# Optimization experiments

Measured on AMD Instinct MI355X. Metric: run time of the kernel, lower is better.

The kernel has to match this reference:

```python
import jax, jax.numpy as jnp
import numpy as np

N = 111          # brain regions
K_POOL = 100     # ceil(0.9 * 111), hard-coded by inter_channel_adj shape
C_ASSIGN = 56    # int(0.5 * 112)
B = 2048
E = 4000

LEFT = np.array([6,5,55,1,98,71,73,77,63,96,79,15,104,4,25,23,41,43,45,17,61,65,59,57,86,21,35,37,39,94,110,3,69,81,84,100,102,106,47,27,75,2,67,19,49,31,33,108,51,53,88,90,92,29,0])
RIGHT = np.array([13,12,54,8,97,70,72,76,62,95,78,14,103,11,24,22,40,42,44,16,60,64,58,56,85,20,34,36,38,93,109,10,68,80,83,99,101,105,46,26,74,9,66,18,48,30,32,107,50,52,87,89,91,28,7])

def _gcn(x, A, W, b):
    # PyG GCNConv: out = D^-1/2 (A + I) D^-1/2 (x W) + b, deg from weighted adj + self loops
    Ah = A + jnp.eye(N, dtype=x.dtype)
    d = Ah.sum(axis=1)
    dis = jnp.where(d > 0, jax.lax.rsqrt(d), 0.0).astype(x.dtype)
    return (dis[:, None] * Ah * dis[None, :]) @ (x @ W) + b

def _forward_batch(features, edge_attr, edge_index, params):
    src, dst = edge_index[0], edge_index[1]
    inL = jnp.zeros((N,), bool).at[jnp.asarray(LEFT)].set(True)
    inR = jnp.zeros((N,), bool).at[jnp.asarray(RIGHT)].set(True)
    # subgraph(): keep edges with both endpoints in hemisphere (masking == removal for weighted GCN)
    ml = (inL[src] & inL[dst]).astype(features.dtype)
    mr = (inR[src] & inR[dst]).astype(features.dtype)
    (W_l1, b_l1, W_r1, b_r1, W_l2, b_l2, W_r2, b_r2, W_g1, b_g1,
     W_rel, b_rel, W_root, W_c0, W_c1, W_c2, b_c) = params
    lrelu = lambda z: jax.nn.leaky_relu(z, 0.01)
    no_diag = 1.0 - jnp.eye(N, dtype=features.dtype)

    def one(x, ew):
        dense = lambda w: jnp.zeros((N, N), x.dtype).at[dst, src].add(w)  # A[target, source]
        A_l, A_r, A_g = dense(ew * ml), dense(ew * mr), dense(ew)
        hl = lrelu(_gcn(x, A_l, W_l1, b_l1))
        hr = lrelu(_gcn(x, A_r, W_r1, b_r1))
        h1 = jnp.zeros((N, 64), x.dtype).at[LEFT].set(hl[LEFT]).at[RIGHT].set(hr[RIGHT])
        hl2 = lrelu(_gcn(h1, A_l, W_l2, b_l2))
        hr2 = lrelu(_gcn(h1, A_r, W_r2, b_r2))
        h2 = jnp.zeros((N, 20), x.dtype).at[LEFT].set(hl2[LEFT]).at[RIGHT].set(hr2[RIGHT])
        h2 = lrelu(_gcn(h2, A_g, W_g1, b_g1))
        # SAGPooling: GraphConv score (aggr=add with edge weights) -> tanh -> top-100
        score = jnp.tanh((A_g @ h2) @ W_rel + b_rel + h2 @ W_root)[:, 0]
        perm = jnp.argsort(-score)[:K_POOL]               # descending-score order (PyG topk)
        pooled = h2[perm] * score[perm][:, None]          # [100, 20]
        # filter_adj: relabel surviving edges into 0..99 (ChebConv still runs on 111 nodes)
        mapping = jnp.full((N,), -1, jnp.int32).at[perm].set(jnp.arange(K_POOL, dtype=jnp.int32))
        ms, mt = mapping[src], mapping[dst]
        keepb = (ms >= 0) & (mt >= 0)
        A_p = jnp.zeros((N, N), x.dtype).at[jnp.where(keepb, mt, 0), jnp.where(keepb, ms, 0)].add(keepb.astype(x.dtype)) * no_diag
        # ChebConv K=3, sym norm, lambda_max=2 -> scaled Laplacian = -D^-1/2 A D^-1/2 (zero diag)
        dC = A_p.sum(axis=0)
        disC = jnp.where(dC > 0, jax.lax.rsqrt(dC), 0.0).astype(x.dtype)
        Lh = -(disC[:, None] * A_p * disC[None, :])
        Tx1 = Lh @ h2
        Tx2 = 2.0 * (Lh @ Tx1) - h2
        ass = jax.nn.softmax(h2 @ W_c0 + Tx1 @ W_c1 + Tx2 @ W_c2 + b_c, axis=-1)  # [111, 56]
        s2 = jax.nn.softmax(ass, axis=-1)  # dense_diff_pool softmaxes again (faithful)
        Hc = s2.T @ h2                     # [56, 20]
        # python loop: rows of ass for nodes in perm with index < 110, ascending node order
        sp = jnp.sort(perm)
        inter = ass[sp] * (sp < 110)[:, None].astype(x.dtype)  # [100, 56]
        return (pooled + inter @ Hc).reshape(1, -1)             # [1, 2000]

    return jax.vmap(one)(features, edge_attr)

def setup_inputs() -> dict:
    key = jax.random.key(0)
    ks = jax.random.split(key, 16)
    w = lambda k, shape: 0.1 * jax.random.normal(k, shape, jnp.float32)
    inp = {
        'features': jax.random.normal(ks[0], (B, N, N), jnp.float32),
        'edge_attr': jax.random.uniform(ks[1], (B, E), jnp.float32),
        'adj': jax.random.uniform(ks[2], (B, N, N), jnp.float32),
        'edge_index': jax.random.randint(ks[3], (2, E), 0, N),
        'W_l1': w(ks[4], (N, 64)), 'b_l1': jnp.zeros((64,), jnp.float32),
        'W_r1': w(ks[5], (N, 64)), 'b_r1': jnp.zeros((64,), jnp.float32),
        'W_l2': w(ks[6], (64, 20)), 'b_l2': jnp.zeros((20,), jnp.float32),
        'W_r2': w(ks[7], (64, 20)), 'b_r2': jnp.zeros((20,), jnp.float32),
        'W_g1': w(ks[8], (20, 20)), 'b_g1': jnp.zeros((20,), jnp.float32),
        'W_rel': w(ks[9], (20, 1)), 'b_rel': jnp.zeros((1,), jnp.float32),
        'W_root': w(ks[10], (20, 1)),
        'W_c0': w(ks[11], (20, C_ASSIGN)), 'W_c1': w(ks[12], (20, C_ASSIGN)),
        'W_c2': w(ks[13], (20, C_ASSIGN)), 'b_c': jnp.zeros((C_ASSIGN,), jnp.float32),
    }
    return inp

def reference(features, edge_attr, adj, edge_index, W_l1, b_l1, W_r1, b_r1, W_l2, b_l2, W_r2, b_r2, W_g1, b_g1, W_rel, b_rel, W_root, W_c0, W_c1, W_c2, b_c):
    params = (W_l1, b_l1, W_r1, b_r1, W_l2, b_l2, W_r2, b_r2, W_g1, b_g1, W_rel, b_rel, W_root, W_c0, W_c1, W_c2, b_c)
    return _forward_batch(features, edge_attr, edge_index, params)
```

## Files before the change

### kernel.cpp

```cpp
#include <hip/hip_runtime.h>
#include <math.h>

#define N    111
#define NR   112
#define NE   4000
#define KP   100
#define APs  104
#define CA   56
#define NT   1024

__device__ __constant__ int d_P2O[112] = {
  6,5,55,1,98,71,73,77,63,96,79,15,104,4,25,23,41,43,45,17,61,65,59,57,86,21,
  35,37,39,94,110,3,69,81,84,100,102,106,47,27,75,2,67,19,49,31,33,108,51,53,
  88,90,92,29,0,
  82,
  13,12,54,8,97,70,72,76,62,95,78,14,103,11,24,22,40,42,44,16,60,64,58,56,85,
  20,34,36,38,93,109,10,68,80,83,99,101,105,46,26,74,9,66,18,48,30,32,107,50,
  52,87,89,91,28,7,
  111};

#define OFF_A 0
#define OFF_B 12544
#define OFF_C 24976
#define OFF_D 32144
#define FSZ   39312

__device__ __forceinline__ float lrelu(float h) { return h > 0.f ? h : 0.01f * h; }

__global__ __launch_bounds__(NT, 1)
void brain_fused(const float* __restrict__ features,
                 const float* __restrict__ edge_attr,
                 const int*   __restrict__ edge_index,
                 const float* __restrict__ Wl1, const float* __restrict__ bl1,
                 const float* __restrict__ Wr1, const float* __restrict__ br1,
                 const float* __restrict__ Wl2, const float* __restrict__ bl2,
                 const float* __restrict__ Wr2, const float* __restrict__ br2,
                 const float* __restrict__ Wg1, const float* __restrict__ bg1,
                 const float* __restrict__ Wrel, const float* __restrict__ brel,
                 const float* __restrict__ Wroot,
                 const float* __restrict__ Wc0, const float* __restrict__ Wc1,
                 const float* __restrict__ Wc2, const float* __restrict__ bc,
                 float* __restrict__ out)
{
    __shared__ __align__(16) float F[FSZ];
    __shared__ float disH[112], disG[112], disC[112], scoreS[112];
    __shared__ int o2rS[112], mapRank[112], permSh[KP], spSh[KP];

    float* Ag   = F + OFF_A;
    float* Ap   = F + OFF_A;
    float* assS = F + OFF_A;
    float* HcS  = F + OFF_A + 6216;
    float* Xs   = F + OFF_B;
    float* W2s  = F + OFF_B;
    float* Wg1s = F + OFF_B + 2560;
    float* TC   = F + OFF_B;
    float* Tx1  = F + OFF_B + 2080;
    float* Tx2  = F + OFF_B + 4080;
    float* TC2  = F + OFF_B + 6160;
    float* s2S  = F + OFF_B;
    float* T64  = F + OFF_C;
    float* T20x = F + OFF_C;
    float* Wcs  = F + OFF_C;
    float* H1   = F + OFF_D;
    float* Wlds = F + OFF_D;
    float* H2   = F + OFF_D;
    float* H2g  = F + OFF_D + 2240;

    const int b    = blockIdx.x;
    const int tid  = threadIdx.x;
    const int lane = tid & 63;
    const int wv   = tid >> 6;
    const float* x = features + (size_t)b * (N * N);

    for (int o = tid; o < 12544; o += NT) Ag[o] = 0.f;
    for (int o = tid; o < 7168;  o += NT) T64[o] = 0.f;
    if (tid < 112) o2rS[d_P2O[tid]] = tid;
    __syncthreads();

    #pragma unroll 2
    for (int e = tid; e < NE; e += NT) {
        int s = o2rS[edge_index[e]];
        int t = o2rS[edge_index[NE + e]];
        atomicAdd(&Ag[t * NR + s], edge_attr[(size_t)b * NE + e]);
    }
    __syncthreads();

    #pragma unroll 2
    for (int o = tid; o < N * NR; o += NT) {
        int r = o / NR, cc = o % NR;
        Xs[o] = (cc < N) ? x[d_P2O[r] * N + cc] : 0.f;
    }
    __syncthreads();

    #pragma unroll 1
    for (int k = 0; k < 7; ++k) {
        int r = wv + 16 * k;
        if (r >= 112) continue;
        if (r == 111) { if (lane == 0) { disH[111] = 0.f; disG[111] = 0.f; } continue; }
        float a0 = Ag[r * NR + lane];
        float a1 = (lane < 48) ? Ag[r * NR + 64 + lane] : 0.f;
        float sG = a0 + a1;
        float sH;
        if (r < 55)       sH = (lane < 55) ? a0 : 0.f;
        else if (r >= 56) sH = ((lane >= 56) ? a0 : 0.f) + ((lane < 47) ? a1 : 0.f);
        else              sH = 0.f;
        #pragma unroll
        for (int m = 1; m < 64; m <<= 1) {
            sG += __shfl_xor(sG, m);
            sH += __shfl_xor(sH, m);
        }
        if (lane == 0) {
            disG[r] = 1.f / sqrtf(sG + 1.f);
            disH[r] = (r == 55) ? 0.f : 1.f / sqrtf(sH + 1.f);
        }
    }
    __syncthreads();

    #pragma unroll 1
    for (int half = 0; half < 2; ++half) {
        const float* W = (half == 0) ? Wl1 : Wr1;
        __syncthreads();
        #pragma unroll 2
        for (int o = tid; o < 1792; o += NT) {
            float4 v = make_float4(0.f, 0.f, 0.f, 0.f);
            if (o < 1776) v = ((const float4*)W)[o];
            ((float4*)Wlds)[o] = v;
        }
        __syncthreads();
        const int rlim  = (half == 0) ? 55 : 111;
        const int rbase = (half == 0) ? wv * 4 : 56 + wv * 4;
        float acc[4] = {0,0,0,0};
        int rr[4];
        #pragma unroll
        for (int u = 0; u < 4; ++u) { int r = rbase + u; rr[u] = (r < rlim) ? r : (rlim - 1); }
        #pragma unroll 1
        for (int j4 = 0; j4 < 28; ++j4) {
            float w0 = Wlds[(4 * j4 + 0) * 64 + lane];
            float w1 = Wlds[(4 * j4 + 1) * 64 + lane];
            float w2 = Wlds[(4 * j4 + 2) * 64 + lane];
            float w3 = Wlds[(4 * j4 + 3) * 64 + lane];
            #pragma unroll
            for (int u = 0; u < 4; ++u) {
                const float4 xv = *(const float4*)&Xs[rr[u] * NR + 4 * j4];
                acc[u] += xv.x * w0 + xv.y * w1 + xv.z * w2 + xv.w * w3;
            }
        }
        #pragma unroll
        for (int u = 0; u < 4; ++u) {
            int r = rbase + u;
            if (r < rlim) T64[r * 64 + lane] = disH[r] * acc[u];
        }
    }
    __syncthreads();

    #pragma unroll 2
    for (int o = tid; o < 1280; o += NT) { W2s[o] = Wl2[o]; W2s[1280 + o] = Wr2[o]; }
    if (tid < 400) Wg1s[tid] = Wg1[tid];
    if (tid >= 448 && tid < 512) H1[55 * 64 + (tid - 448)] = 0.f;
    __syncthreads();

    #pragma unroll 1
    for (int half = 0; half < 2; ++half) {
        const int  rbase = half == 0 ? wv * 4 : 56 + wv * 4;
        const int  rlim  = half == 0 ? 55 : 111;
        const int  jb    = half == 0 ? 0 : 56;
        const float* bb  = half == 0 ? bl1 : br1;
        float acc[4] = {0,0,0,0};
        int rr[4];
        #pragma unroll
        for (int u = 0; u < 4; ++u) { int r = rbase + u; rr[u] = (r < rlim) ? r : (rlim - 1); }
        #pragma unroll 2
        for (int j4 = 0; j4 < 14; ++j4) {
            float t0 = T64[(jb + 4 * j4 + 0) * 64 + lane];
            float t1 = T64[(jb + 4 * j4 + 1) * 64 + lane];
            float t2 = T64[(jb + 4 * j4 + 2) * 64 + lane];
            float t3 = T64[(jb + 4 * j4 + 3) * 64 + lane];
            #pragma unroll
            for (int u = 0; u < 4; ++u) {
                const float4 a4 = *(const float4*)&Ag[rr[u] * NR + jb + 4 * j4];
                acc[u] += a4.x * t0 + a4.y * t1 + a4.z * t2 + a4.w * t3;
            }
        }
        float bv = bb[lane];
        #pragma unroll
        for (int u = 0; u < 4; ++u) {
            int r = rbase + u;
            if (r < rlim && r != 55)
                H1[r * 64 + lane] = lrelu(disH[r] * (acc[u] + T64[r * 64 + lane]) + bv);
        }
    }
    __syncthreads();

    for (int o = tid; o < 560; o += NT) {
        int i = o / 5, c0 = (o % 5) * 4;
        if (i == 111) { *(float4*)&T20x[i * 20 + c0] = make_float4(0.f,0.f,0.f,0.f); continue; }
        const float* W2 = (i < 56) ? W2s : (W2s + 1280);
        const float4* h4 = (const float4*)(H1 + i * 64);
        float4 acc = make_float4(0.f,0.f,0.f,0.f);
        #pragma unroll 2
        for (int k4 = 0; k4 < 16; ++k4) {
            float4 h = h4[k4];
            float4 w0 = *(const float4*)&W2[(4 * k4 + 0) * 20 + c0];
            float4 w1 = *(const float4*)&W2[(4 * k4 + 1) * 20 + c0];
            float4 w2 = *(const float4*)&W2[(4 * k4 + 2) * 20 + c0];
            float4 w3 = *(const float4*)&W2[(4 * k4 + 3) * 20 + c0];
            acc.x += h.x * w0.x + h.y * w1.x + h.z * w2.x + h.w * w3.x;
            acc.y += h.x * w0.y + h.y * w1.y + h.z * w2.y + h.w * w3.y;
            acc.z += h.x * w0.z + h.y * w1.z + h.z * w2.z + h.w * w3.z;
            acc.w += h.x * w0.w + h.y * w1.w + h.z * w2.w + h.w * w3.w;
        }
        float d = disH[i];
        *(float4*)&T20x[i * 20 + c0] = make_float4(d*acc.x, d*acc.y, d*acc.z, d*acc.w);
    }
    __syncthreads();

    for (int o = tid; o < 555; o += NT) {
        int i = o / 5, c0 = (o % 5) * 4;
        if (i == 55) { *(float4*)&H2[i * 20 + c0] = make_float4(0.f,0.f,0.f,0.f); continue; }
        int jb = (i < 56) ? 0 : 56;
        float4 acc = make_float4(0.f,0.f,0.f,0.f);
        #pragma unroll 2
        for (int j4 = 0; j4 < 14; ++j4) {
            float4 a  = *(const float4*)&Ag[i * NR + jb + 4 * j4];
            float4 t0 = *(const float4*)&T20x[(jb + 4 * j4 + 0) * 20 + c0];
            float4 t1 = *(const float4*)&T20x[(jb + 4 * j4 + 1) * 20 + c0];
            float4 t2 = *(const float4*)&T20x[(jb + 4 * j4 + 2) * 20 + c0];
            float4 t3 = *(const float4*)&T20x[(jb + 4 * j4 + 3) * 20 + c0];
            acc.x += a.x * t0.x + a.y * t1.x + a.z * t2.x + a.w * t3.x;
            acc.y += a.x * t0.y + a.y * t1.y + a.z * t2.y + a.w * t3.y;
            acc.z += a.x * t0.z + a.y * t1.z + a.z * t2.z + a.w * t3.z;
            acc.w += a.x * t0.w + a.y * t1.w + a.z * t2.w + a.w * t3.w;
        }
        float4 self = *(const float4*)&T20x[i * 20 + c0];
        float4 bv = *(const float4*)&((i < 56) ? bl2 : br2)[c0];
        float dh = disH[i];
        float4 r;
        r.x = lrelu(dh * (acc.x + self.x) + bv.x);
        r.y = lrelu(dh * (acc.y + self.y) + bv.y);
        r.z = lrelu(dh * (acc.z + self.z) + bv.z);
        r.w = lrelu(dh * (acc.w + self.w) + bv.w);
        *(float4*)&H2[i * 20 + c0] = r;
    }
    __syncthreads();

    for (int o = tid; o < 560; o += NT) {
        int i = o / 5, c0 = (o % 5) * 4;
        if (i == 111) { *(float4*)&T20x[i * 20 + c0] = make_float4(0.f,0.f,0.f,0.f); continue; }
        float4 acc = make_float4(0.f,0.f,0.f,0.f);
        #pragma unroll 4
        for (int k = 0; k < 20; ++k) {
            float h = H2[i * 20 + k];
            float4 w = *(const float4*)&Wg1s[k * 20 + c0];
            acc.x += h * w.x; acc.y += h * w.y; acc.z += h * w.z; acc.w += h * w.w;
        }
        float d = disG[i];
        *(float4*)&T20x[i * 20 + c0] = make_float4(d*acc.x, d*acc.y, d*acc.z, d*acc.w);
    }
    __syncthreads();

    for (int o = tid; o < 555; o += NT) {
        int i = o / 5, c0 = (o % 5) * 4;
        float4 acc = make_float4(0.f,0.f,0.f,0.f);
        #pragma unroll 2
        for (int j4 = 0; j4 < 28; ++j4) {
            float4 a  = *(const float4*)&Ag[i * NR + 4 * j4];
            float4 t0 = *(const float4*)&T20x[(4 * j4 + 0) * 20 + c0];
            float4 t1 = *(const float4*)&T20x[(4 * j4 + 1) * 20 + c0];
            float4 t2 = *(const float4*)&T20x[(4 * j4 + 2) * 20 + c0];
            float4 t3 = *(const float4*)&T20x[(4 * j4 + 3) * 20 + c0];
            acc.x += a.x * t0.x + a.y * t1.x + a.z * t2.x + a.w * t3.x;
            acc.y += a.x * t0.y + a.y * t1.y + a.z * t2.y + a.w * t3.y;
            acc.z += a.x * t0.z + a.y * t1.z + a.z * t2.z + a.w * t3.z;
            acc.w += a.x * t0.w + a.y * t1.w + a.z * t2.w + a.w * t3.w;
        }
        float4 self = *(const float4*)&T20x[i * 20 + c0];
        float4 bv = *(const float4*)&bg1[c0];
        float dg = disG[i];
        float4 r;
        r.x = lrelu(dg * (acc.x + self.x) + bv.x);
        r.y = lrelu(dg * (acc.y + self.y) + bv.y);
        r.z = lrelu(dg * (acc.z + self.z) + bv.z);
        r.w = lrelu(dg * (acc.w + self.w) + bv.w);
        *(float4*)&H2g[i * 20 + c0] = r;
    }
    __syncthreads();

    if (tid < 112) {
        if (tid == 111) { disC[111] = 0.f; scoreS[111] = 0.f; }
        else {
            float uu = 0.f, vv = 0.f;
            #pragma unroll 4
            for (int c = 0; c < 20; ++c) {
                float h = H2g[tid * 20 + c];
                uu += h * Wrel[c];
                vv += h * Wroot[c];
            }
            disC[tid] = uu; scoreS[tid] = vv;
        }
    }
    __syncthreads();

    {
        float brel0 = brel[0];
        #pragma unroll 1
        for (int k = 0; k < 7; ++k) {
            int r = wv + 16 * k;
            if (r >= N) continue;
            float p = Ag[r * NR + lane] * disC[lane];
            if (lane < 48) p += Ag[r * NR + 64 + lane] * disC[64 + lane];
            #pragma unroll
            for (int m = 1; m < 64; m <<= 1) p += __shfl_xor(p, m);
            if (lane == 0) scoreS[r] = tanhf(p + scoreS[r] + brel0);
        }
    }
    __syncthreads();

    if (tid < N) {
        float si = scoreS[tid];
        int oi = d_P2O[tid];
        int r = 0;
        #pragma unroll 4
        for (int j = 0; j < N; ++j) {
            float sj = scoreS[j];
            r += (sj > si || (sj == si && d_P2O[j] < oi)) ? 1 : 0;
        }
        mapRank[tid] = (r < KP) ? r : -1;
        if (r < KP) permSh[r] = tid;
    }
    if (tid == N) mapRank[111] = -1;
    for (int o = tid; o < KP * APs; o += NT) Ap[o] = 0.f;
    __syncthreads();
    if (tid < N && mapRank[tid] >= 0) {
        int oi = d_P2O[tid], pos = 0;
        #pragma unroll 4
        for (int j = 0; j < N; ++j) pos += (mapRank[j] >= 0 && d_P2O[j] < oi) ? 1 : 0;
        spSh[pos] = tid;
    }
    __syncthreads();
    #pragma unroll 2
    for (int e = tid; e < NE; e += NT) {
        int sr = o2rS[edge_index[e]];
        int tr = o2rS[edge_index[NE + e]];
        int ms = mapRank[sr], mt = mapRank[tr];
        if (ms >= 0 && mt >= 0 && ms != mt) atomicAdd(&Ap[mt * APs + ms], 1.f);
    }
    __syncthreads();

    if (tid < APs) {
        if (tid >= KP) disC[tid] = 0.f;
        else {
            float d0 = 0.f, d1 = 0.f;
            #pragma unroll 4
            for (int a = 0; a < KP; a += 2) {
                d0 += Ap[a * APs + tid];
                d1 += Ap[(a + 1) * APs + tid];
            }
            float d = d0 + d1;
            disC[tid] = (d > 0.f) ? 1.f / sqrtf(d) : 0.f;
        }
    }
    __syncthreads();

    for (int o = tid; o < 520; o += NT) {
        int bq = o / 5, c0 = (o % 5) * 4;
        float4 h = *(const float4*)&H2g[o2rS[bq] * 20 + c0];
        float d = disC[bq];
        *(float4*)&TC[bq * 20 + c0] = make_float4(d*h.x, d*h.y, d*h.z, d*h.w);
    }
    #pragma unroll 2
    for (int o = tid; o < 1120; o += NT) {
        Wcs[o] = Wc0[o]; Wcs[1120 + o] = Wc1[o]; Wcs[2240 + o] = Wc2[o];
    }
    if (tid < 80) TC2[2000 + tid] = 0.f;
    __syncthreads();

    for (int o = tid; o < 500; o += NT) {
        int a = o / 5, c0 = (o % 5) * 4;
        float4 acc = make_float4(0.f,0.f,0.f,0.f);
        #pragma unroll 2
        for (int j4 = 0; j4 < 26; ++j4) {
            float4 av = *(const float4*)&Ap[a * APs + 4 * j4];
            float4 t0 = *(const float4*)&TC[(4 * j4 + 0) * 20 + c0];
            float4 t1 = *(const float4*)&TC[(4 * j4 + 1) * 20 + c0];
            float4 t2 = *(const float4*)&TC[(4 * j4 + 2) * 20 + c0];
            float4 t3 = *(const float4*)&TC[(4 * j4 + 3) * 20 + c0];
            acc.x += av.x * t0.x + av.y * t1.x + av.z * t2.x + av.w * t3.x;
            acc.y += av.x * t0.y + av.y * t1.y + av.z * t2.y + av.w * t3.y;
            acc.z += av.x * t0.z + av.y * t1.z + av.z * t2.z + av.w * t3.z;
            acc.w += av.x * t0.w + av.y * t1.w + av.z * t2.w + av.w * t3.w;
        }
        float d = disC[a];
        float4 t = make_float4(-d*acc.x, -d*acc.y, -d*acc.z, -d*acc.w);
        *(float4*)&Tx1[a * 20 + c0] = t;
        *(float4*)&TC2[a * 20 + c0] = make_float4(d*t.x, d*t.y, d*t.z, d*t.w);
    }
    __syncthreads();

    for (int o = tid; o < 500; o += NT) {
        int a = o / 5, c0 = (o % 5) * 4;
        float4 acc = make_float4(0.f,0.f,0.f,0.f);
        #pragma unroll 2
        for (int j4 = 0; j4 < 26; ++j4) {
            float4 av = *(const float4*)&Ap[a * APs + 4 * j4];
            float4 t0 = *(const float4*)&TC2[(4 * j4 + 0) * 20 + c0];
            float4 t1 = *(const float4*)&TC2[(4 * j4 + 1) * 20 + c0];
            float4 t2 = *(const float4*)&TC2[(4 * j4 + 2) * 20 + c0];
            float4 t3 = *(const float4*)&TC2[(4 * j4 + 3) * 20 + c0];
            acc.x += av.x * t0.x + av.y * t1.x + av.z * t2.x + av.w * t3.x;
            acc.y += av.x * t0.y + av.y * t1.y + av.z * t2.y + av.w * t3.y;
            acc.z += av.x * t0.z + av.y * t1.z + av.z * t2.z + av.w * t3.z;
            acc.w += av.x * t0.w + av.y * t1.w + av.z * t2.w + av.w * t3.w;
        }
        float d2 = -2.f * disC[a];
        float4 h = *(const float4*)&H2g[o2rS[a] * 20 + c0];
        *(float4*)&Tx2[a * 20 + c0] =
            make_float4(d2*acc.x - h.x, d2*acc.y - h.y, d2*acc.z - h.z, d2*acc.w - h.w);
    }
    __syncthreads();

    {
        float bcv = (lane < CA) ? bc[lane] : 0.f;
        const int base = wv * 7;
        float acc[7] = {0,0,0,0,0,0,0};
        int ho[7], txo[7], in7[7];
        #pragma unroll
        for (int u = 0; u < 7; ++u) {
            int i = base + u;
            int ic = (i < N) ? i : (N - 1);
            ho[u]  = o2rS[ic] * 20;
            in7[u] = (ic < KP) ? 1 : 0;
            txo[u] = ((ic < KP) ? ic : 0) * 20;
        }
        #pragma unroll 1
        for (int k = 0; k < 20; ++k) {
            float w0 = Wcs[k * CA + lane];
            float w1 = Wcs[1120 + k * CA + lane];
            float w2 = Wcs[2240 + k * CA + lane];
            #pragma unroll
            for (int u = 0; u < 7; ++u) {
                float h  = H2g[ho[u] + k];
                float t1 = in7[u] ? Tx1[txo[u] + k] : 0.f;
                float t2 = in7[u] ? Tx2[txo[u] + k] : -h;
                acc[u] += h * w0 + t1 * w1 + t2 * w2;
            }
        }
        #pragma unroll
        for (int u = 0; u < 7; ++u) {
            int i = base + u;
            if (i < N && lane < CA) assS[i * CA + lane] = acc[u] + bcv;
        }
    }
    __syncthreads();

    #pragma unroll 1
    for (int k = 0; k < 7; ++k) {
        int r = wv + 16 * k;
        if (r >= N) continue;
        float v = (lane < CA) ? assS[r * CA + lane] : -3.4e38f;
        float m = v;
        #pragma unroll
        for (int s = 1; s < 64; s <<= 1) m = fmaxf(m, __shfl_xor(m, s));
        float e = (lane < CA) ? expf(v - m) : 0.f;
        float sum = e;
        #pragma unroll
        for (int s = 1; s < 64; s <<= 1) sum += __shfl_xor(sum, s);
        float p1 = e / sum;
        float m2 = (lane < CA) ? p1 : -3.4e38f;
        #pragma unroll
        for (int s = 1; s < 64; s <<= 1) m2 = fmaxf(m2, __shfl_xor(m2, s));
        float e2 = (lane < CA) ? expf(p1 - m2) : 0.f;
        float sum2 = e2;
        #pragma unroll
        for (int s = 1; s < 64; s <<= 1) sum2 += __shfl_xor(sum2, s);
        if (lane < CA) {
            assS[r * CA + lane] = p1;
            s2S[r * CA + lane]  = e2 / sum2;
        }
    }
    __syncthreads();

    for (int o = tid; o < 280; o += NT) {
        int q = o / 5, c0 = (o % 5) * 4;
        float4 acc = make_float4(0.f,0.f,0.f,0.f);
        #pragma unroll 2
        for (int r = 0; r < N; ++r) {
            float s = s2S[d_P2O[r] * CA + q];
            float4 h = *(const float4*)&H2g[r * 20 + c0];
            acc.x += s * h.x; acc.y += s * h.y; acc.z += s * h.z; acc.w += s * h.w;
        }
        *(float4*)&HcS[q * 20 + c0] = acc;
    }
    __syncthreads();

    for (int o = tid; o < 500; o += NT) {
        int k = o / 5, c0 = (o % 5) * 4;
        int rp = permSh[k];
        float sc = scoreS[rp];
        float4 hq = *(const float4*)&H2g[rp * 20 + c0];
        float4 v = make_float4(sc*hq.x, sc*hq.y, sc*hq.z, sc*hq.w);
        int oi = d_P2O[spSh[k]];
        if (oi < 110) {
            float4 acc = make_float4(0.f,0.f,0.f,0.f);
            #pragma unroll 4
            for (int q = 0; q < CA; ++q) {
                float s = assS[oi * CA + q];
                float4 h = *(const float4*)&HcS[q * 20 + c0];
                acc.x += s * h.x; acc.y += s * h.y; acc.z += s * h.z; acc.w += s * h.w;
            }
            v.x += acc.x; v.y += acc.y; v.z += acc.z; v.w += acc.w;
        }
        *(float4*)&out[(size_t)b * (KP * 20) + k * 20 + c0] = v;
    }
}

extern "C" void kernel_launch(void* const* d_in, const int* in_sizes, int n_in,
                              void* d_out, int out_size, void* d_ws, size_t ws_size,
                              hipStream_t stream) {
    const float* features   = (const float*)d_in[0];
    const float* edge_attr  = (const float*)d_in[1];
    const int*   edge_index = (const int*)d_in[3];
    const float* Wl1 = (const float*)d_in[4];
    const float* bl1 = (const float*)d_in[5];
    const float* Wr1 = (const float*)d_in[6];
    const float* br1 = (const float*)d_in[7];
    const float* Wl2 = (const float*)d_in[8];
    const float* bl2 = (const float*)d_in[9];
    const float* Wr2 = (const float*)d_in[10];
    const float* br2 = (const float*)d_in[11];
    const float* Wg1 = (const float*)d_in[12];
    const float* bg1 = (const float*)d_in[13];
    const float* Wrel = (const float*)d_in[14];
    const float* brel = (const float*)d_in[15];
    const float* Wroot = (const float*)d_in[16];
    const float* Wc0 = (const float*)d_in[17];
    const float* Wc1 = (const float*)d_in[18];
    const float* Wc2 = (const float*)d_in[19];
    const float* bc  = (const float*)d_in[20];
    float* out = (float*)d_out;

    int B = in_sizes[0] / (N * N);
    brain_fused<<<dim3(B), dim3(NT), 0, stream>>>(
        features, edge_attr, edge_index,
        Wl1, bl1, Wr1, br1, Wl2, bl2, Wr2, br2, Wg1, bg1,
        Wrel, brel, Wroot, Wc0, Wc1, Wc2, bc, out);
}
```

Baseline: 822.0 us.

## Merge hemisphere GCN passes and fuse double softmax into assignment GEMM

Both hemisphere weight matrices are now loaded into LDS together with the feature tile, so a single pass has 16 waves each computing 7 rows (left waves use Wl1, right waves use Wr1). This replaces the two serialized half-passes and their extra barriers, and the second-layer aggregation is restructured the same way. The double softmax on the assignment matrix now runs in registers straight after the assignment GEMM, removing an LDS round trip and a barrier. The cost is more accumulators per wave and therefore higher register pressure, plus an added barrier before the T64 overwrite, since T64 now also holds the right-hemisphere weights.

Result: faster. 761.5 us (-7.4%).

```diff
diff --git a/kernel.cpp b/kernel.cpp
--- a/kernel.cpp
+++ b/kernel.cpp
@@ -73,7 +73,6 @@
     const float* x = features + (size_t)b * (N * N);
 
     for (int o = tid; o < 12544; o += NT) Ag[o] = 0.f;
-    for (int o = tid; o < 7168;  o += NT) T64[o] = 0.f;
     if (tid < 112) o2rS[d_P2O[tid]] = tid;
     __syncthreads();
 
@@ -89,6 +88,13 @@
     for (int o = tid; o < N * NR; o += NT) {
         int r = o / NR, cc = o % NR;
         Xs[o] = (cc < N) ? x[d_P2O[r] * N + cc] : 0.f;
+    }
+    #pragma unroll 2
+    for (int o = tid; o < 1792; o += NT) {
+        float4 vl = make_float4(0.f,0.f,0.f,0.f), vr = vl;
+        if (o < 1776) { vl = ((const float4*)Wl1)[o]; vr = ((const float4*)Wr1)[o]; }
+        ((float4*)Wlds)[o] = vl;
+        ((float4*)T64)[o]  = vr;
     }
     __syncthreads();
 
@@ -116,40 +122,30 @@
     }
     __syncthreads();
 
-    #pragma unroll 1
-    for (int half = 0; half < 2; ++half) {
-        const float* W = (half == 0) ? Wl1 : Wr1;
-        __syncthreads();
-        #pragma unroll 2
-        for (int o = tid; o < 1792; o += NT) {
-            float4 v = make_float4(0.f, 0.f, 0.f, 0.f);
-            if (o < 1776) v = ((const float4*)W)[o];
-            ((float4*)Wlds)[o] = v;
-        }
-        __syncthreads();
-        const int rlim  = (half == 0) ? 55 : 111;
-        const int rbase = (half == 0) ? wv * 4 : 56 + wv * 4;
-        float acc[4] = {0,0,0,0};
-        int rr[4];
-        #pragma unroll
-        for (int u = 0; u < 4; ++u) { int r = rbase + u; rr[u] = (r < rlim) ? r : (rlim - 1); }
+    {
+        const bool left = (wv < 8);
+        const float* W = left ? Wlds : T64;
+        const int rbase = wv * 7;
+        float acc[7] = {0,0,0,0,0,0,0};
         #pragma unroll 1
         for (int j4 = 0; j4 < 28; ++j4) {
-            float w0 = Wlds[(4 * j4 + 0) * 64 + lane];
-            float w1 = Wlds[(4 * j4 + 1) * 64 + lane];
-            float w2 = Wlds[(4 * j4 + 2) * 64 + lane];
-            float w3 = Wlds[(4 * j4 + 3) * 64 + lane];
-            #pragma unroll
-            for (int u = 0; u < 4; ++u) {
-                const float4 xv = *(const float4*)&Xs[rr[u] * NR + 4 * j4];
+            float w0 = W[(4 * j4 + 0) * 64 + lane];
+            float w1 = W[(4 * j4 + 1) * 64 + lane];
+            float w2 = W[(4 * j4 + 2) * 64 + lane];
+            float w3 = W[(4 * j4 + 3) * 64 + lane];
+            #pragma unroll
+            for (int u = 0; u < 7; ++u) {
+                const float4 xv = *(const float4*)&Xs[(rbase + u) * NR + 4 * j4];
                 acc[u] += xv.x * w0 + xv.y * w1 + xv.z * w2 + xv.w * w3;
             }
         }
+        __syncthreads();
         #pragma unroll
-        for (int u = 0; u < 4; ++u) {
+        for (int u = 0; u < 7; ++u) {
             int r = rbase + u;
-            if (r < rlim) T64[r * 64 + lane] = disH[r] * acc[u];
-        }
+            if (r < 111) T64[r * 64 + lane] = disH[r] * acc[u];
+        }
+        if (wv == 15 && lane < 64) T64[111 * 64 + lane] = 0.f;
     }
     __syncthreads();
 
@@ -159,16 +155,12 @@
     if (tid >= 448 && tid < 512) H1[55 * 64 + (tid - 448)] = 0.f;
     __syncthreads();
 
-    #pragma unroll 1
-    for (int half = 0; half < 2; ++half) {
-        const int  rbase = half == 0 ? wv * 4 : 56 + wv * 4;
-        const int  rlim  = half == 0 ? 55 : 111;
-        const int  jb    = half == 0 ? 0 : 56;
-        const float* bb  = half == 0 ? bl1 : br1;
-        float acc[4] = {0,0,0,0};
-        int rr[4];
-        #pragma unroll
-        for (int u = 0; u < 4; ++u) { int r = rbase + u; rr[u] = (r < rlim) ? r : (rlim - 1); }
+    {
+        const bool left = (wv < 8);
+        const int  rbase = wv * 7;
+        const int  jb    = left ? 0 : 56;
+        const float* bb  = left ? bl1 : br1;
+        float acc[7] = {0,0,0,0,0,0,0};
         #pragma unroll 2
         for (int j4 = 0; j4 < 14; ++j4) {
             float t0 = T64[(jb + 4 * j4 + 0) * 64 + lane];
@@ -176,16 +168,16 @@
             float t2 = T64[(jb + 4 * j4 + 2) * 64 + lane];
             float t3 = T64[(jb + 4 * j4 + 3) * 64 + lane];
             #pragma unroll
-            for (int u = 0; u < 4; ++u) {
-                const float4 a4 = *(const float4*)&Ag[rr[u] * NR + jb + 4 * j4];
+            for (int u = 0; u < 7; ++u) {
+                const float4 a4 = *(const float4*)&Ag[(rbase + u) * NR + jb + 4 * j4];
                 acc[u] += a4.x * t0 + a4.y * t1 + a4.z * t2 + a4.w * t3;
             }
         }
         float bv = bb[lane];
         #pragma unroll
-        for (int u = 0; u < 4; ++u) {
+        for (int u = 0; u < 7; ++u) {
             int r = rbase + u;
-            if (r < rlim && r != 55)
+            if (r < 111 && r != 55)
                 H1[r * 64 + lane] = lrelu(disH[r] * (acc[u] + T64[r * 64 + lane]) + bv);
         }
     }
@@ -444,37 +436,35 @@
                 acc[u] += h * w0 + t1 * w1 + t2 * w2;
             }
         }
+        float p1v[7], s2v[7];
+        #pragma unroll 1
+        for (int u = 0; u < 7; ++u) {
+            float v = (lane < CA) ? acc[u] + bcv : -3.4e38f;
+            float m = v;
+            #pragma unroll
+            for (int s = 1; s < 64; s <<= 1) m = fmaxf(m, __shfl_xor(m, s));
+            float e = (lane < CA) ? expf(v - m) : 0.f;
+            float sum = e;
+            #pragma unroll
+            for (int s = 1; s < 64; s <<= 1) sum += __shfl_xor(sum, s);
+            float p1 = e / sum;
+            float m2 = (lane < CA) ? p1 : -3.4e38f;
+            #pragma unroll
+            for (int s = 1; s < 64; s <<= 1) m2 = fmaxf(m2, __shfl_xor(m2, s));
+            float e2 = (lane < CA) ? expf(p1 - m2) : 0.f;
+            float sum2 = e2;
+            #pragma unroll
+            for (int s = 1; s < 64; s <<= 1) sum2 += __shfl_xor(sum2, s);
+            p1v[u] = p1; s2v[u] = e2 / sum2;
+        }
+        __syncthreads();
         #pragma unroll
         for (int u = 0; u < 7; ++u) {
             int i = base + u;
-            if (i < N && lane < CA) assS[i * CA + lane] = acc[u] + bcv;
-        }
-    }
-    __syncthreads();
-
-    #pragma unroll 1
-    for (int k = 0; k < 7; ++k) {
-        int r = wv + 16 * k;
-        if (r >= N) continue;
-        float v = (lane < CA) ? assS[r * CA + lane] : -3.4e38f;
-        float m = v;
-        #pragma unroll
-        for (int s = 1; s < 64; s <<= 1) m = fmaxf(m, __shfl_xor(m, s));
-        float e = (lane < CA) ? expf(v - m) : 0.f;
-        float sum = e;
-        #pragma unroll
-        for (int s = 1; s < 64; s <<= 1) sum += __shfl_xor(sum, s);
-        float p1 = e / sum;
-        float m2 = (lane < CA) ? p1 : -3.4e38f;
-        #pragma unroll
-        for (int s = 1; s < 64; s <<= 1) m2 = fmaxf(m2, __shfl_xor(m2, s));
-        float e2 = (lane < CA) ? expf(p1 - m2) : 0.f;
-        float sum2 = e2;
-        #pragma unroll
-        for (int s = 1; s < 64; s <<= 1) sum2 += __shfl_xor(sum2, s);
-        if (lane < CA) {
-            assS[r * CA + lane] = p1;
-            s2S[r * CA + lane]  = e2 / sum2;
+            if (i < N && lane < CA) {
+                assS[i * CA + lane] = p1v[u];
+                s2S[i * CA + lane]  = s2v[u];
+            }
         }
     }
     __syncthreads();
```
